# Kernel tuning notes

Measured on AMD Instinct MI355X. Metric: run time of the kernel, lower is better.

Reference implementation:

```python
import jax, jax.numpy as jnp
import numpy as np

B, S, D, H = 2, 2048, 1024, 16
DK = D // H

def setup_inputs() -> dict:
    key = jax.random.key(0)
    ks = jax.random.split(key, 11)
    scale = 1.0 / np.sqrt(D)
    inp = {
        'Q': jax.random.normal(ks[0], (B, S, D), jnp.float32),
        'K': jax.random.normal(ks[1], (B, S, D), jnp.float32),
        'V': jax.random.normal(ks[2], (B, S, D), jnp.float32),
        'Wq': jax.random.normal(ks[3], (D, D), jnp.float32) * scale,
        'bq': jax.random.normal(ks[4], (D,), jnp.float32) * 0.01,
        'Wk': jax.random.normal(ks[5], (D, D), jnp.float32) * scale,
        'bk': jax.random.normal(ks[6], (D,), jnp.float32) * 0.01,
        'Wv': jax.random.normal(ks[7], (D, D), jnp.float32) * scale,
        'bv': jax.random.normal(ks[8], (D,), jnp.float32) * 0.01,
        'Wo': jax.random.normal(ks[9], (D, D), jnp.float32) * scale,
        'bo': jax.random.normal(ks[10], (D,), jnp.float32) * 0.01,
    }
    return inp

def reference(Q, K, V, Wq, bq, Wk, bk, Wv, bv, Wo, bo):
    bs = Q.shape[0]
    # projections (torch Linear: x @ W.T + b), reshape to [b, h, s, d_k]
    q = (Q @ Wq.T + bq).reshape(bs, -1, H, DK).transpose(0, 2, 1, 3)
    k = (K @ Wk.T + bk).reshape(bs, -1, H, DK).transpose(0, 2, 1, 3)
    v = (V @ Wv.T + bv).reshape(bs, -1, H, DK).transpose(0, 2, 1, 3)
    # scaled dot-product attention (no mask, dropout p=0)
    scores = jnp.einsum('bhqd,bhkd->bhqk', q, k) / np.sqrt(DK).astype(np.float32)
    attn = jax.nn.softmax(scores, axis=-1)
    ctx = jnp.einsum('bhqk,bhkd->bhqd', attn, v)
    concat = ctx.transpose(0, 2, 1, 3).reshape(bs, -1, D)
    return concat @ Wo.T + bo
```

## Files before the change

### kernel.cpp

```cpp
#include <hip/hip_runtime.h>
#include <hip/hip_bf16.h>
#include <stdint.h>

#define B_  2
#define S_  2048
#define D_  1024
#define H_  16
#define DK_ 64
#define M_  (B_ * S_)

#define QSCALE 0.18033688011112042f

typedef __attribute__((ext_vector_type(4)))  float f32x4;
typedef __attribute__((ext_vector_type(16))) float f32x16;
typedef __attribute__((ext_vector_type(8)))  short bf16x8;

__device__ __forceinline__ unsigned short f2bf(float f) {
    union { float f; unsigned u; } a; a.f = f;
    unsigned u = a.u;
    unsigned r = (u + 0x7fffu + ((u >> 16) & 1u)) >> 16;
    return (unsigned short)r;
}
__device__ __forceinline__ unsigned pk2(float lo, float hi) {
    union { float f; unsigned u; } a, b; a.f = lo; b.f = hi;
    unsigned ra = a.u + 0x7fffu + ((a.u >> 16) & 1u);
    unsigned rb = b.u + 0x7fffu + ((b.u >> 16) & 1u);
    return __builtin_amdgcn_perm(rb, ra, 0x07060302u);
}
__device__ __forceinline__ unsigned pk2f(float lo, float hi) {
    union { float f; unsigned u; } a, b; a.f = lo; b.f = hi;
    return __builtin_amdgcn_perm(b.u + 0x8000u, a.u + 0x8000u, 0x07060302u);
}

__device__ __forceinline__ void gload16(const void* g, void* l) {
    __builtin_amdgcn_global_load_lds(
        (const __attribute__((address_space(1))) void*)g,
        (__attribute__((address_space(3))) void*)l, 16, 0, 0);
}

__global__ __launch_bounds__(256) void cvt_all(
    const float* __restrict__ p0, const float* __restrict__ p1,
    const float* __restrict__ p2, const float* __restrict__ p3,
    const float* __restrict__ p4, const float* __restrict__ p5,
    const float* __restrict__ p6,
    unsigned short* __restrict__ o0, unsigned short* __restrict__ o1,
    unsigned short* __restrict__ o2, unsigned short* __restrict__ o3,
    unsigned short* __restrict__ o4, unsigned short* __restrict__ o5,
    unsigned short* __restrict__ o6) {
    const int y = blockIdx.y;
    if (y >= 3 && blockIdx.x >= 512) return;
    const float* in = (y == 0) ? p0 : (y == 1) ? p1 : (y == 2) ? p2 :
                      (y == 3) ? p3 : (y == 4) ? p4 : (y == 5) ? p5 : p6;
    unsigned short* out = (y == 0) ? o0 : (y == 1) ? o1 : (y == 2) ? o2 :
                          (y == 3) ? o3 : (y == 4) ? o4 : (y == 5) ? o5 : o6;
    const int i = blockIdx.x * 256 + threadIdx.x;
    const float4* p = (const float4*)in + (size_t)i * 2;
    float4 u = p[0], v = p[1];
    union { unsigned us[4]; bf16x8 v; } o;
    o.us[0] = pk2(u.x, u.y); o.us[1] = pk2(u.z, u.w);
    o.us[2] = pk2(v.x, v.y); o.us[3] = pk2(v.z, v.w);
    *((bf16x8*)out + i) = o.v;
}

__device__ __forceinline__ void gemm128_core(const unsigned short* __restrict__ A,
                                             const unsigned short* __restrict__ Bw,
                                             char* sm,
                                             int brow, int bcol, f32x4 (&acc)[4][4]) {
    constexpr int K = D_;
    const int t = threadIdx.x;
    const int l = t & 63;
    const int l15 = l & 15, l4 = l >> 4;
    const int wr = (t >> 6) >> 1, wc = (t >> 6) & 1;

    const unsigned short* Ap = A + (size_t)(brow + (t >> 2)) * K + (t & 3) * 8;
    const unsigned short* Bp = Bw + (size_t)(bcol + (t >> 2)) * K + (t & 3) * 8;

    {
        char* d = sm + t * 16;
        gload16(Ap, d);
        gload16(Ap + 64 * K, d + 4096);
        gload16(Bp, d + 8192);
        gload16(Bp + 64 * K, d + 12288);
    }
    __syncthreads();

    unsigned sbuf = 0;
    for (int k0 = 0; k0 < K; k0 += 32) {
        if (k0 + 32 < K) {
            char* d = sm + (sbuf ^ 16384u) + t * 16;
            gload16(Ap + k0 + 32, d);
            gload16(Ap + 64 * K + k0 + 32, d + 4096);
            gload16(Bp + k0 + 32, d + 8192);
            gload16(Bp + 64 * K + k0 + 32, d + 12288);
        }

        const char* Ab = sm + sbuf;
        bf16x8 af[4], bfv[4];
#pragma unroll
        for (int m = 0; m < 4; m++)
            af[m] = *(const bf16x8*)(Ab + (wr * 64 + m * 16 + l15) * 64 + l4 * 16);
#pragma unroll
        for (int n = 0; n < 4; n++)
            bfv[n] = *(const bf16x8*)(Ab + 8192 + (wc * 64 + n * 16 + l15) * 64 + l4 * 16);
#pragma unroll
        for (int m = 0; m < 4; m++)
#pragma unroll
            for (int n = 0; n < 4; n++)
                acc[m][n] = __builtin_amdgcn_mfma_f32_16x16x32_bf16(af[m], bfv[n],
                                                                    acc[m][n], 0, 0, 0);

        if (k0 + 32 < K) __syncthreads();
        sbuf ^= 16384u;
    }
}

__global__ __launch_bounds__(256) void gemm_qkv(
    const unsigned short* __restrict__ xq, const unsigned short* __restrict__ xk,
    const unsigned short* __restrict__ xv,
    const unsigned short* __restrict__ wq, const unsigned short* __restrict__ wk,
    const unsigned short* __restrict__ wv,
    const float* __restrict__ bq, const float* __restrict__ bk,
    const float* __restrict__ bv,
    unsigned short* __restrict__ oq, unsigned short* __restrict__ ok,
    unsigned short* __restrict__ ov) {
    __shared__ char sm[32768];

    const int bid = blockIdx.x;
    const int wg = (bid & 7) * 96 + (bid >> 3);
    const int bx = wg & 7, by = (wg >> 3) & 31, z = wg >> 8;

    const unsigned short* A  = (z == 0) ? xq : (z == 1) ? xk : xv;
    const unsigned short* Bw = (z == 0) ? wq : (z == 1) ? wk : wv;
    const float* bias        = (z == 0) ? bq : (z == 1) ? bk : bv;
    unsigned short* out      = (z == 0) ? oq : (z == 1) ? ok : ov;

    const int brow = by * 128;
    const int bcol = bx * 128;
    const f32x4 zf = {0.0f, 0.0f, 0.0f, 0.0f};
    f32x4 acc[4][4];
#pragma unroll
    for (int i = 0; i < 4; i++)
#pragma unroll
        for (int j = 0; j < 4; j++) acc[i][j] = zf;

    gemm128_core(A, Bw, sm, brow, bcol, acc);

    const int t = threadIdx.x;
    const int l = t & 63;
    const int l15 = l & 15, l4 = l >> 4;
    const int wr = (t >> 6) >> 1, wc = (t >> 6) & 1;
    const float scale = (z == 0) ? QSCALE : 1.0f;

#pragma unroll
    for (int n = 0; n < 4; n++) {
        const int col = bcol + wc * 64 + n * 16 + l15;
        const float bia = bias[col];
        const int h = col >> 6, dk = col & 63;
#pragma unroll
        for (int m = 0; m < 4; m++) {
            const int row0 = brow + wr * 64 + m * 16 + l4 * 4;
            const int b = row0 >> 11, s0 = row0 & (S_ - 1);
            if (z != 2) {
#pragma unroll
                for (int r = 0; r < 4; r++) {
                    float v = (acc[m][n][r] + bia) * scale;
                    out[((size_t)((b * H_ + h) * S_ + (s0 + r))) * DK_ + dk] = f2bf(v);
                }
            } else {
                const int st_ = s0 >> 7, sl = s0 & 127;
                const int g = (sl >> 6) & 1, c = (sl >> 4) & 3;
                const int j2 = (sl >> 2) & 3;
                const int sig = ((j2 & 1) << 1) | (j2 >> 1);
                uint2 o;
                o.x = pk2(acc[m][n][0] + bia, acc[m][n][1] + bia);
                o.y = pk2(acc[m][n][2] + bia, acc[m][n][3] + bia);
                *(uint2*)((char*)out +
                          (((((size_t)(b * H_ + h) * 16 + st_) * 2 + g) * 4 + c) * 64 + dk) * 32 +
                          sig * 8) = o;
            }
        }
    }
}

__global__ __launch_bounds__(256) void gemm_out(const unsigned short* __restrict__ A,
                                                const unsigned short* __restrict__ Bw,
                                                const float* __restrict__ bias,
                                                float* __restrict__ out) {
    __shared__ char sm[32768];

    const int bid = blockIdx.x;
    const int wg = (bid & 7) * 32 + (bid >> 3);
    const int bx = wg & 7, by = wg >> 3;

    const int brow = by * 128;
    const int bcol = bx * 128;
    const f32x4 zf = {0.0f, 0.0f, 0.0f, 0.0f};
    f32x4 acc[4][4];
#pragma unroll
    for (int i = 0; i < 4; i++)
#pragma unroll
        for (int j = 0; j < 4; j++) acc[i][j] = zf;

    gemm128_core(A, Bw, sm, brow, bcol, acc);

    const int t = threadIdx.x;
    const int l = t & 63;
    const int l15 = l & 15, l4 = l >> 4;
    const int wr = (t >> 6) >> 1, wc = (t >> 6) & 1;
#pragma unroll
    for (int n = 0; n < 4; n++) {
        const int col = bcol + wc * 64 + n * 16 + l15;
        const float bia = bias[col];
#pragma unroll
        for (int m = 0; m < 4; m++) {
            const int row0 = brow + wr * 64 + m * 16 + l4 * 4;
#pragma unroll
            for (int r = 0; r < 4; r++)
                out[(size_t)(row0 + r) * D_ + col] = acc[m][n][r] + bia;
        }
    }
}

__global__ __launch_bounds__(512, 4) void attn_kernel(const unsigned short* __restrict__ qh,
                                                      const unsigned short* __restrict__ kh,
                                                      const unsigned short* __restrict__ vimg,
                                                      unsigned short* __restrict__ ctx) {
    __shared__ unsigned short smem[2][16384];
    char* smb = (char*)smem;

    const int t = threadIdx.x;
    const int w = t >> 6, l = t & 63;
    const int l31 = l & 31, hi = l >> 5;
    const int hi16 = hi * 16;
    const int grp = w >> 2;
    const int qs  = w & 3;

    const int bid = blockIdx.x;
    const int bh = (bid & 7) * 4 + ((bid >> 3) & 3);
    const int qt = bid >> 5;
    const int b = bh >> 4, h = bh & 15;

    const unsigned short* qg = qh + (size_t)bh * S_ * DK_;
    const unsigned short* kg = kh + (size_t)bh * S_ * DK_;

    const int q0 = qt * 128 + qs * 32;

    bf16x8 qf[4];
#pragma unroll
    for (int kc = 0; kc < 4; kc++)
        qf[kc] = *(const bf16x8*)(qg + (size_t)(q0 + l31) * DK_ + kc * 16 + hi * 8);

    const f32x16 zf16 = {0.0f};
    f32x16 acc0 = zf16, acc1 = zf16;
    float lpart = 0.0f;

    const int kc_ = t >> 7, key_ = (t >> 1) & 63, hi_ = t & 1;
    const unsigned short* ksrc = kg + key_ * DK_ + kc_ * 16 + hi_ * 8;
    const unsigned short* vsrc = vimg + (size_t)bh * (16 * 8192) + t * 8;

    {
        char* kd = smb + t * 16;
        gload16(ksrc, kd);
        gload16(ksrc + 4096, kd + 8192);
        gload16(vsrc, kd + 16384);
        gload16(vsrc + 4096, kd + 16384 + 8192);
        ksrc += 8192; vsrc += 8192;
    }
    __syncthreads();

    unsigned roff = grp * 8192 + l31 * 32 + hi16;
    unsigned pd = 32768 + (unsigned)t * 16;

    for (int j = 0; j < 16; ++j) {
        if (j < 15) {
            gload16(ksrc, smb + pd);
            gload16(ksrc + 4096, smb + pd + 8192);
            gload16(vsrc, smb + pd + 16384);
            gload16(vsrc + 4096, smb + pd + 16384 + 8192);
            ksrc += 8192; vsrc += 8192;
        }

        const char* Kb = smb + roff;

        f32x16 st0, st1;
        __builtin_amdgcn_s_setprio(1);
        {
            bf16x8 k0 = *(const bf16x8*)(Kb);
            bf16x8 k1 = *(const bf16x8*)(Kb + 1024);
            st0 = __builtin_amdgcn_mfma_f32_32x32x16_bf16(k0, qf[0], zf16, 0, 0, 0);
            st1 = __builtin_amdgcn_mfma_f32_32x32x16_bf16(k1, qf[0], zf16, 0, 0, 0);
        }
#pragma unroll
        for (int kc = 1; kc < 4; kc++) {
            bf16x8 k0 = *(const bf16x8*)(Kb + kc * 2048);
            bf16x8 k1 = *(const bf16x8*)(Kb + kc * 2048 + 1024);
            st0 = __builtin_amdgcn_mfma_f32_32x32x16_bf16(k0, qf[kc], st0, 0, 0, 0);
            st1 = __builtin_amdgcn_mfma_f32_32x32x16_bf16(k1, qf[kc], st1, 0, 0, 0);
        }
        __builtin_amdgcn_s_setprio(0);

#pragma unroll
        for (int i = 0; i < 16; i++) st0[i] = __builtin_amdgcn_exp2f(st0[i]);
#pragma unroll
        for (int i = 0; i < 16; i++) st1[i] = __builtin_amdgcn_exp2f(st1[i]);

        float sv[8];
#pragma unroll
        for (int i = 0; i < 8; i++) sv[i] = (st0[i] + st0[i + 8]) + (st1[i] + st1[i + 8]);
#pragma unroll
        for (int s = 4; s >= 1; s >>= 1)
#pragma unroll
            for (int i = 0; i < s; i++) sv[i] += sv[i + s];
        lpart += sv[0];

        bf16x8 pf[4];
        {
            union { unsigned u[4]; bf16x8 v; } pu;
            pu.u[0] = pk2f(st0[0], st0[1]);   pu.u[1] = pk2f(st0[2], st0[3]);
            pu.u[2] = pk2f(st0[4], st0[5]);   pu.u[3] = pk2f(st0[6], st0[7]);
            pf[0] = pu.v;
            pu.u[0] = pk2f(st0[8], st0[9]);   pu.u[1] = pk2f(st0[10], st0[11]);
            pu.u[2] = pk2f(st0[12], st0[13]); pu.u[3] = pk2f(st0[14], st0[15]);
            pf[1] = pu.v;
            pu.u[0] = pk2f(st1[0], st1[1]);   pu.u[1] = pk2f(st1[2], st1[3]);
            pu.u[2] = pk2f(st1[4], st1[5]);   pu.u[3] = pk2f(st1[6], st1[7]);
            pf[2] = pu.v;
            pu.u[0] = pk2f(st1[8], st1[9]);   pu.u[1] = pk2f(st1[10], st1[11]);
            pu.u[2] = pk2f(st1[12], st1[13]); pu.u[3] = pk2f(st1[14], st1[15]);
            pf[3] = pu.v;
        }

        const char* Vb = smb + roff;
        __builtin_amdgcn_s_setprio(1);
#pragma unroll
        for (int c = 0; c < 4; c++) {
            bf16x8 v0 = *(const bf16x8*)(Vb + 16384 + c * 2048);
            bf16x8 v1 = *(const bf16x8*)(Vb + 16384 + c * 2048 + 1024);
            acc0 = __builtin_amdgcn_mfma_f32_32x32x16_bf16(v0, pf[c], acc0, 0, 0, 0);
            acc1 = __builtin_amdgcn_mfma_f32_32x32x16_bf16(v1, pf[c], acc1, 0, 0, 0);
        }
        __builtin_amdgcn_s_setprio(0);

        if (j < 15) __syncthreads();
        roff ^= 32768;
        pd ^= 32768;
    }

    lpart += __shfl_xor(lpart, 32);
    __syncthreads();
    char* ab = smb + qs * 8192 + l31 * 256;
    const int msw = (l31 & 7) << 4;
    if (grp == 1) {
#pragma unroll
        for (int jj = 0; jj < 4; jj++) {
            f32x4 x0 = {acc0[4 * jj], acc0[4 * jj + 1], acc0[4 * jj + 2], acc0[4 * jj + 3]};
            f32x4 x1 = {acc1[4 * jj], acc1[4 * jj + 1], acc1[4 * jj + 2], acc1[4 * jj + 3]};
            *(f32x4*)(ab + ((jj * 32 + hi16) ^ msw)) = x0;
            *(f32x4*)(ab + (128 + ((jj * 32 + hi16) ^ msw))) = x1;
        }
        if (hi == 0)
            *(float*)(smb + 32768 + qs * 128 + l31 * 4) = lpart;
    }
    __syncthreads();
    if (grp == 0) {
        const float lB = *(const float*)(smb + 32768 + qs * 128 + l31 * 4);
        const float inv = 1.0f / (lpart + lB);
        unsigned short* op = ctx + ((size_t)b * S_ + (q0 + l31)) * D_ + h * 64;
#pragma unroll
        for (int jj = 0; jj < 4; jj++) {
            f32x4 b0 = *(const f32x4*)(ab + ((jj * 32 + hi16) ^ msw));
            f32x4 b1 = *(const f32x4*)(ab + (128 + ((jj * 32 + hi16) ^ msw)));
            uint2 o;
            o.x = pk2f((acc0[4 * jj + 0] + b0[0]) * inv, (acc0[4 * jj + 1] + b0[1]) * inv);
            o.y = pk2f((acc0[4 * jj + 2] + b0[2]) * inv, (acc0[4 * jj + 3] + b0[3]) * inv);
            *(uint2*)(op + jj * 8 + hi * 4) = o;
            o.x = pk2f((acc1[4 * jj + 0] + b1[0]) * inv, (acc1[4 * jj + 1] + b1[1]) * inv);
            o.y = pk2f((acc1[4 * jj + 2] + b1[2]) * inv, (acc1[4 * jj + 3] + b1[3]) * inv);
            *(uint2*)(op + 32 + jj * 8 + hi * 4) = o;
        }
    }
}

extern "C" void kernel_launch(void* const* d_in, const int* in_sizes, int n_in,
                              void* d_out, int out_size, void* d_ws, size_t ws_size,
                              hipStream_t stream) {
    const float* Q  = (const float*)d_in[0];
    const float* K  = (const float*)d_in[1];
    const float* V  = (const float*)d_in[2];
    const float* Wq = (const float*)d_in[3];
    const float* bq = (const float*)d_in[4];
    const float* Wk = (const float*)d_in[5];
    const float* bk = (const float*)d_in[6];
    const float* Wv = (const float*)d_in[7];
    const float* bv = (const float*)d_in[8];
    const float* Wo = (const float*)d_in[9];
    const float* bo = (const float*)d_in[10];

    const size_t NX = (size_t)M_ * D_;
    const size_t NW = (size_t)D_ * D_;

    unsigned short* ws = (unsigned short*)d_ws;
    unsigned short* xq  = ws; ws += NX;
    unsigned short* xk  = ws; ws += NX;
    unsigned short* xv  = ws; ws += NX;
    unsigned short* wqb = ws; ws += NW;
    unsigned short* wkb = ws; ws += NW;
    unsigned short* wvb = ws; ws += NW;
    unsigned short* wob = ws; ws += NW;
    unsigned short* qhb = ws; ws += NX;
    unsigned short* khb = ws; ws += NX;
    unsigned short* vip = ws; ws += NX;
    unsigned short* ctx = ws; ws += NX;

    cvt_all<<<dim3(2048, 7), 256, 0, stream>>>(Q, K, V, Wq, Wk, Wv, Wo,
                                               xq, xk, xv, wqb, wkb, wvb, wob);

    gemm_qkv<<<dim3(768), 256, 0, stream>>>(
        xq, xk, xv, wqb, wkb, wvb, bq, bk, bv, qhb, khb, vip);

    attn_kernel<<<dim3(512), 512, 0, stream>>>(qhb, khb, vip, ctx);

    gemm_out<<<dim3(256), 256, 0, stream>>>(ctx, wob, bo, (float*)d_out);
}
```

Before: 111.4 us.

## Rewrite QKV projection GEMM with 256x256 tiles and staged pipelined loads

```diff
diff --git a/kernel.cpp b/kernel.cpp
--- a/kernel.cpp
+++ b/kernel.cpp
@@ -62,6 +62,153 @@
     *((bf16x8*)out + i) = o.v;
 }
 
+template <int R, int C>
+__device__ __forceinline__ void qkv_phase(const char* bb, unsigned rA0, unsigned rB0,
+                                          f32x4 (&aq)[4][2]) {
+    bf16x8 af[4];
+    bf16x8 bf2[2];
+#pragma unroll
+    for (int m = 0; m < 4; m++)
+        af[m] = *(const bf16x8*)(bb + rA0 + R * 8192 + m * 256);
+#pragma unroll
+    for (int n = 0; n < 2; n++)
+        bf2[n] = *(const bf16x8*)(bb + rB0 + C * 8192 + n * 256);
+    __builtin_amdgcn_s_setprio(1);
+#pragma unroll
+    for (int m = 0; m < 4; m++)
+#pragma unroll
+        for (int n = 0; n < 2; n++)
+            aq[m][n] = __builtin_amdgcn_mfma_f32_16x16x32_bf16(af[m], bf2[n],
+                                                               aq[m][n], 0, 0, 0);
+    __builtin_amdgcn_s_setprio(0);
+}
+
+__global__ __launch_bounds__(512, 2) void gemm_qkv(
+    const unsigned short* __restrict__ xq, const unsigned short* __restrict__ xk,
+    const unsigned short* __restrict__ xv,
+    const unsigned short* __restrict__ wq, const unsigned short* __restrict__ wk,
+    const unsigned short* __restrict__ wv,
+    const float* __restrict__ bq, const float* __restrict__ bk,
+    const float* __restrict__ bv,
+    unsigned short* __restrict__ oq, unsigned short* __restrict__ ok,
+    unsigned short* __restrict__ ov) {
+    constexpr int K = D_;
+    __shared__ char sm[65536];
+    char* smd = sm;
+
+    const int bid = blockIdx.x;
+    const int wg = (bid & 7) * 24 + (bid >> 3);
+    const int z = wg >> 6;
+    const int rz = wg & 63;
+    const int by = rz >> 2, bx = rz & 3;
+    const int brow = by * 256, bcol = bx * 256;
+
+    const unsigned short* A  = (z == 0) ? xq : (z == 1) ? xk : xv;
+    const unsigned short* Bw = (z == 0) ? wq : (z == 1) ? wk : wv;
+    const float* bias        = (z == 0) ? bq : (z == 1) ? bk : bv;
+    unsigned short* out      = (z == 0) ? oq : (z == 1) ? ok : ov;
+
+    const int t = threadIdx.x;
+    const int l = t & 63, w = t >> 6;
+    const int l15 = l & 15, l4 = l >> 4;
+    const int wr2 = w >> 2, wc2 = w & 3;
+
+    const f32x4 zf = {0.0f, 0.0f, 0.0f, 0.0f};
+    f32x4 acc0[4][2], acc1[4][2], acc2[4][2], acc3[4][2];
+#pragma unroll
+    for (int m = 0; m < 4; m++)
+#pragma unroll
+        for (int n = 0; n < 2; n++) {
+            acc0[m][n] = zf; acc1[m][n] = zf; acc2[m][n] = zf; acc3[m][n] = zf;
+        }
+
+    const unsigned short* ApT = A + (size_t)(brow + (t & 127)) * K + (t >> 7) * 8;
+    const unsigned short* BpT = Bw + (size_t)(bcol + (t & 127)) * K + (t >> 7) * 8;
+    const unsigned dln = (unsigned)t * 16;
+
+    auto STAGE_A = [&](int h, int k0, unsigned buf) {
+        gload16(ApT + (size_t)h * 128 * K + k0, smd + buf + h * 8192 + dln);
+    };
+    auto STAGE_B = [&](int h, int k0, unsigned buf) {
+        gload16(BpT + (size_t)h * 128 * K + k0, smd + buf + 16384 + h * 8192 + dln);
+    };
+
+    const unsigned rA0 = (unsigned)((l4 * 128 + wr2 * 64 + l15) * 16);
+    const unsigned rB0 = 16384u + (unsigned)((l4 * 128 + wc2 * 32 + l15) * 16);
+
+    STAGE_A(0, 0, 0u); STAGE_B(0, 0, 0u); STAGE_A(1, 0, 0u); STAGE_B(1, 0, 0u);
+
+    constexpr int NT = K / 32;
+    for (int kt = 0; kt < NT; ++kt) {
+        const unsigned cur = (kt & 1) ? 32768u : 0u;
+        const unsigned nb = cur ^ 32768u;
+        const char* bb = smd + cur;
+        if (kt + 1 < NT) {
+            const int k1 = (kt + 1) * 32;
+            STAGE_A(0, k1, nb);
+            asm volatile("s_waitcnt vmcnt(3)\n\ts_barrier" ::: "memory");
+            __builtin_amdgcn_sched_barrier(0);
+            qkv_phase<0, 0>(bb, rA0, rB0, acc0);
+            STAGE_B(0, k1, nb);
+            asm volatile("s_waitcnt vmcnt(3)\n\ts_barrier" ::: "memory");
+            __builtin_amdgcn_sched_barrier(0);
+            qkv_phase<1, 0>(bb, rA0, rB0, acc1);
+            STAGE_A(1, k1, nb);
+            asm volatile("s_waitcnt vmcnt(3)\n\ts_barrier" ::: "memory");
+            __builtin_amdgcn_sched_barrier(0);
+            qkv_phase<0, 1>(bb, rA0, rB0, acc2);
+            STAGE_B(1, k1, nb);
+            asm volatile("s_barrier" ::: "memory");
+            __builtin_amdgcn_sched_barrier(0);
+            qkv_phase<1, 1>(bb, rA0, rB0, acc3);
+        } else {
+            asm volatile("s_waitcnt vmcnt(0)\n\ts_barrier" ::: "memory");
+            __builtin_amdgcn_sched_barrier(0);
+            qkv_phase<0, 0>(bb, rA0, rB0, acc0);
+            qkv_phase<1, 0>(bb, rA0, rB0, acc1);
+            qkv_phase<0, 1>(bb, rA0, rB0, acc2);
+            qkv_phase<1, 1>(bb, rA0, rB0, acc3);
+        }
+    }
+
+    const float scale = (z == 0) ? QSCALE : 1.0f;
+    auto epi = [&](f32x4 (&aq)[4][2], int R, int C) {
+#pragma unroll
+        for (int n = 0; n < 2; n++) {
+            const int col = bcol + C * 128 + wc2 * 32 + n * 16 + l15;
+            const float bia = bias[col];
+            const int h = col >> 6, dk = col & 63;
+#pragma unroll
+            for (int m = 0; m < 4; m++) {
+                const int row0 = brow + R * 128 + wr2 * 64 + m * 16 + l4 * 4;
+                const int b = row0 >> 11, s0 = row0 & (S_ - 1);
+                if (z != 2) {
+#pragma unroll
+                    for (int r = 0; r < 4; r++) {
+                        float v = (aq[m][n][r] + bia) * scale;
+                        out[((size_t)((b * H_ + h) * S_ + (s0 + r))) * DK_ + dk] = f2bf(v);
+                    }
+                } else {
+                    const int st_ = s0 >> 7, sl = s0 & 127;
+                    const int g = (sl >> 6) & 1, c = (sl >> 4) & 3;
+                    const int j2 = (sl >> 2) & 3;
+                    const int sig = ((j2 & 1) << 1) | (j2 >> 1);
+                    uint2 o;
+                    o.x = pk2(aq[m][n][0] + bia, aq[m][n][1] + bia);
+                    o.y = pk2(aq[m][n][2] + bia, aq[m][n][3] + bia);
+                    *(uint2*)((char*)out +
+                              (((((size_t)(b * H_ + h) * 16 + st_) * 2 + g) * 4 + c) * 64 + dk) * 32 +
+                              sig * 8) = o;
+                }
+            }
+        }
+    };
+    epi(acc0, 0, 0);
+    epi(acc1, 1, 0);
+    epi(acc2, 0, 1);
+    epi(acc3, 1, 1);
+}
+
 __device__ __forceinline__ void gemm128_core(const unsigned short* __restrict__ A,
                                              const unsigned short* __restrict__ Bw,
                                              char* sm,
@@ -111,74 +258,6 @@
 
         if (k0 + 32 < K) __syncthreads();
         sbuf ^= 16384u;
-    }
-}
-
-__global__ __launch_bounds__(256) void gemm_qkv(
-    const unsigned short* __restrict__ xq, const unsigned short* __restrict__ xk,
-    const unsigned short* __restrict__ xv,
-    const unsigned short* __restrict__ wq, const unsigned short* __restrict__ wk,
-    const unsigned short* __restrict__ wv,
-    const float* __restrict__ bq, const float* __restrict__ bk,
-    const float* __restrict__ bv,
-    unsigned short* __restrict__ oq, unsigned short* __restrict__ ok,
-    unsigned short* __restrict__ ov) {
-    __shared__ char sm[32768];
-
-    const int bid = blockIdx.x;
-    const int wg = (bid & 7) * 96 + (bid >> 3);
-    const int bx = wg & 7, by = (wg >> 3) & 31, z = wg >> 8;
-
-    const unsigned short* A  = (z == 0) ? xq : (z == 1) ? xk : xv;
-    const unsigned short* Bw = (z == 0) ? wq : (z == 1) ? wk : wv;
-    const float* bias        = (z == 0) ? bq : (z == 1) ? bk : bv;
-    unsigned short* out      = (z == 0) ? oq : (z == 1) ? ok : ov;
-
-    const int brow = by * 128;
-    const int bcol = bx * 128;
-    const f32x4 zf = {0.0f, 0.0f, 0.0f, 0.0f};
-    f32x4 acc[4][4];
-#pragma unroll
-    for (int i = 0; i < 4; i++)
-#pragma unroll
-        for (int j = 0; j < 4; j++) acc[i][j] = zf;
-
-    gemm128_core(A, Bw, sm, brow, bcol, acc);
-
-    const int t = threadIdx.x;
-    const int l = t & 63;
-    const int l15 = l & 15, l4 = l >> 4;
-    const int wr = (t >> 6) >> 1, wc = (t >> 6) & 1;
-    const float scale = (z == 0) ? QSCALE : 1.0f;
-
-#pragma unroll
-    for (int n = 0; n < 4; n++) {
-        const int col = bcol + wc * 64 + n * 16 + l15;
-        const float bia = bias[col];
-        const int h = col >> 6, dk = col & 63;
-#pragma unroll
-        for (int m = 0; m < 4; m++) {
-            const int row0 = brow + wr * 64 + m * 16 + l4 * 4;
-            const int b = row0 >> 11, s0 = row0 & (S_ - 1);
-            if (z != 2) {
-#pragma unroll
-                for (int r = 0; r < 4; r++) {
-                    float v = (acc[m][n][r] + bia) * scale;
-                    out[((size_t)((b * H_ + h) * S_ + (s0 + r))) * DK_ + dk] = f2bf(v);
-                }
-            } else {
-                const int st_ = s0 >> 7, sl = s0 & 127;
-                const int g = (sl >> 6) & 1, c = (sl >> 4) & 3;
-                const int j2 = (sl >> 2) & 3;
-                const int sig = ((j2 & 1) << 1) | (j2 >> 1);
-                uint2 o;
-                o.x = pk2(acc[m][n][0] + bia, acc[m][n][1] + bia);
-                o.y = pk2(acc[m][n][2] + bia, acc[m][n][3] + bia);
-                *(uint2*)((char*)out +
-                          (((((size_t)(b * H_ + h) * 16 + st_) * 2 + g) * 4 + c) * 64 + dk) * 32 +
-                          sig * 8) = o;
-            }
-        }
     }
 }
 
@@ -415,7 +494,7 @@
     cvt_all<<<dim3(2048, 7), 256, 0, stream>>>(Q, K, V, Wq, Wk, Wv, Wo,
                                                xq, xk, xv, wqb, wkb, wvb, wob);
 
-    gemm_qkv<<<dim3(768), 256, 0, stream>>>(
+    gemm_qkv<<<dim3(192), 512, 0, stream>>>(
         xq, xk, xv, wqb, wkb, wvb, bq, bk, bv, qhb, khb, vip);
 
     attn_kernel<<<dim3(512), 512, 0, stream>>>(qhb, khb, vip, ctx);
```

New measurement: 118.5 us. +6.4%, slower.

## Fuse fp32-to-bf16 conversion into GEMM tile loads and drop conversion kernel

Applied to the files above, without the earlier changes.

```diff
diff --git a/kernel.cpp b/kernel.cpp
--- a/kernel.cpp
+++ b/kernel.cpp
@@ -38,61 +38,76 @@
         (__attribute__((address_space(3))) void*)l, 16, 0, 0);
 }
 
-__global__ __launch_bounds__(256) void cvt_all(
-    const float* __restrict__ p0, const float* __restrict__ p1,
-    const float* __restrict__ p2, const float* __restrict__ p3,
-    const float* __restrict__ p4, const float* __restrict__ p5,
-    const float* __restrict__ p6,
-    unsigned short* __restrict__ o0, unsigned short* __restrict__ o1,
-    unsigned short* __restrict__ o2, unsigned short* __restrict__ o3,
-    unsigned short* __restrict__ o4, unsigned short* __restrict__ o5,
-    unsigned short* __restrict__ o6) {
-    const int y = blockIdx.y;
-    if (y >= 3 && blockIdx.x >= 512) return;
-    const float* in = (y == 0) ? p0 : (y == 1) ? p1 : (y == 2) ? p2 :
-                      (y == 3) ? p3 : (y == 4) ? p4 : (y == 5) ? p5 : p6;
-    unsigned short* out = (y == 0) ? o0 : (y == 1) ? o1 : (y == 2) ? o2 :
-                          (y == 3) ? o3 : (y == 4) ? o4 : (y == 5) ? o5 : o6;
-    const int i = blockIdx.x * 256 + threadIdx.x;
-    const float4* p = (const float4*)in + (size_t)i * 2;
-    float4 u = p[0], v = p[1];
-    union { unsigned us[4]; bf16x8 v; } o;
-    o.us[0] = pk2(u.x, u.y); o.us[1] = pk2(u.z, u.w);
-    o.us[2] = pk2(v.x, v.y); o.us[3] = pk2(v.z, v.w);
-    *((bf16x8*)out + i) = o.v;
-}
-
-__device__ __forceinline__ void gemm128_core(const unsigned short* __restrict__ A,
-                                             const unsigned short* __restrict__ Bw,
-                                             char* sm,
-                                             int brow, int bcol, f32x4 (&acc)[4][4]) {
+__device__ __forceinline__ bf16x8 pack8(const float4& a, const float4& b) {
+    union { unsigned u[4]; bf16x8 v; } p;
+    p.u[0] = pk2(a.x, a.y); p.u[1] = pk2(a.z, a.w);
+    p.u[2] = pk2(b.x, b.y); p.u[3] = pk2(b.z, b.w);
+    return p.v;
+}
+
+__global__ __launch_bounds__(256) void gemm_qkv(
+    const float* __restrict__ xq, const float* __restrict__ xk,
+    const float* __restrict__ xv,
+    const float* __restrict__ wq, const float* __restrict__ wk,
+    const float* __restrict__ wv,
+    const float* __restrict__ bq, const float* __restrict__ bk,
+    const float* __restrict__ bv,
+    unsigned short* __restrict__ oq, unsigned short* __restrict__ ok,
+    unsigned short* __restrict__ ov) {
     constexpr int K = D_;
+    __shared__ char sm[32768];
+
+    const int bid = blockIdx.x;
+    const int wg = (bid & 7) * 96 + (bid >> 3);
+    const int bx = wg & 7, by = (wg >> 3) & 31, z = wg >> 8;
+
+    const float* A  = (z == 0) ? xq : (z == 1) ? xk : xv;
+    const float* Bw = (z == 0) ? wq : (z == 1) ? wk : wv;
+    const float* bias = (z == 0) ? bq : (z == 1) ? bk : bv;
+    unsigned short* out = (z == 0) ? oq : (z == 1) ? ok : ov;
+
+    const int brow = by * 128;
+    const int bcol = bx * 128;
+    const f32x4 zf = {0.0f, 0.0f, 0.0f, 0.0f};
+    f32x4 acc[4][4];
+#pragma unroll
+    for (int i = 0; i < 4; i++)
+#pragma unroll
+        for (int j = 0; j < 4; j++) acc[i][j] = zf;
+
     const int t = threadIdx.x;
     const int l = t & 63;
     const int l15 = l & 15, l4 = l >> 4;
     const int wr = (t >> 6) >> 1, wc = (t >> 6) & 1;
 
-    const unsigned short* Ap = A + (size_t)(brow + (t >> 2)) * K + (t & 3) * 8;
-    const unsigned short* Bp = Bw + (size_t)(bcol + (t >> 2)) * K + (t & 3) * 8;
-
-    {
-        char* d = sm + t * 16;
-        gload16(Ap, d);
-        gload16(Ap + 64 * K, d + 4096);
-        gload16(Bp, d + 8192);
-        gload16(Bp + 64 * K, d + 12288);
-    }
+    const float* Ap0 = A + (size_t)(brow + (t >> 2)) * K + (t & 3) * 8;
+    const float* Ap1 = Ap0 + (size_t)64 * K;
+    const float* Bp0 = Bw + (size_t)(bcol + (t >> 2)) * K + (t & 3) * 8;
+    const float* Bp1 = Bp0 + (size_t)64 * K;
+
+    float4 r0a, r0b, r1a, r1b, r2a, r2b, r3a, r3b;
+    auto LOADREG = [&](int k0) {
+        r0a = *(const float4*)(Ap0 + k0); r0b = *(const float4*)(Ap0 + k0 + 4);
+        r1a = *(const float4*)(Ap1 + k0); r1b = *(const float4*)(Ap1 + k0 + 4);
+        r2a = *(const float4*)(Bp0 + k0); r2b = *(const float4*)(Bp0 + k0 + 4);
+        r3a = *(const float4*)(Bp1 + k0); r3b = *(const float4*)(Bp1 + k0 + 4);
+    };
+    auto CVTWRITE = [&](unsigned buf) {
+        char* d = sm + buf + t * 16;
+        *(bf16x8*)(d)         = pack8(r0a, r0b);
+        *(bf16x8*)(d + 4096)  = pack8(r1a, r1b);
+        *(bf16x8*)(d + 8192)  = pack8(r2a, r2b);
+        *(bf16x8*)(d + 12288) = pack8(r3a, r3b);
+    };
+
+    LOADREG(0);
+    CVTWRITE(0u);
     __syncthreads();
 
     unsigned sbuf = 0;
     for (int k0 = 0; k0 < K; k0 += 32) {
-        if (k0 + 32 < K) {
-            char* d = sm + (sbuf ^ 16384u) + t * 16;
-            gload16(Ap + k0 + 32, d);
-            gload16(Ap + 64 * K + k0 + 32, d + 4096);
-            gload16(Bp + k0 + 32, d + 8192);
-            gload16(Bp + 64 * K + k0 + 32, d + 12288);
-        }
+        const bool nx = (k0 + 32 < K);
+        if (nx) LOADREG(k0 + 32);
 
         const char* Ab = sm + sbuf;
         bf16x8 af[4], bfv[4];
@@ -109,48 +124,14 @@
                 acc[m][n] = __builtin_amdgcn_mfma_f32_16x16x32_bf16(af[m], bfv[n],
                                                                     acc[m][n], 0, 0, 0);
 
-        if (k0 + 32 < K) __syncthreads();
+        if (nx) {
+            CVTWRITE(sbuf ^ 16384u);
+            __syncthreads();
+        }
         sbuf ^= 16384u;
     }
-}
-
-__global__ __launch_bounds__(256) void gemm_qkv(
-    const unsigned short* __restrict__ xq, const unsigned short* __restrict__ xk,
-    const unsigned short* __restrict__ xv,
-    const unsigned short* __restrict__ wq, const unsigned short* __restrict__ wk,
-    const unsigned short* __restrict__ wv,
-    const float* __restrict__ bq, const float* __restrict__ bk,
-    const float* __restrict__ bv,
-    unsigned short* __restrict__ oq, unsigned short* __restrict__ ok,
-    unsigned short* __restrict__ ov) {
-    __shared__ char sm[32768];
-
-    const int bid = blockIdx.x;
-    const int wg = (bid & 7) * 96 + (bid >> 3);
-    const int bx = wg & 7, by = (wg >> 3) & 31, z = wg >> 8;
-
-    const unsigned short* A  = (z == 0) ? xq : (z == 1) ? xk : xv;
-    const unsigned short* Bw = (z == 0) ? wq : (z == 1) ? wk : wv;
-    const float* bias        = (z == 0) ? bq : (z == 1) ? bk : bv;
-    unsigned short* out      = (z == 0) ? oq : (z == 1) ? ok : ov;
-
-    const int brow = by * 128;
-    const int bcol = bx * 128;
-    const f32x4 zf = {0.0f, 0.0f, 0.0f, 0.0f};
-    f32x4 acc[4][4];
-#pragma unroll
-    for (int i = 0; i < 4; i++)
-#pragma unroll
-        for (int j = 0; j < 4; j++) acc[i][j] = zf;
-
-    gemm128_core(A, Bw, sm, brow, bcol, acc);
-
-    const int t = threadIdx.x;
-    const int l = t & 63;
-    const int l15 = l & 15, l4 = l >> 4;
-    const int wr = (t >> 6) >> 1, wc = (t >> 6) & 1;
+
     const float scale = (z == 0) ? QSCALE : 1.0f;
-
 #pragma unroll
     for (int n = 0; n < 4; n++) {
         const int col = bcol + wc * 64 + n * 16 + l15;
@@ -183,9 +164,10 @@
 }
 
 __global__ __launch_bounds__(256) void gemm_out(const unsigned short* __restrict__ A,
-                                                const unsigned short* __restrict__ Bw,
+                                                const float* __restrict__ Bw,
                                                 const float* __restrict__ bias,
                                                 float* __restrict__ out) {
+    constexpr int K = D_;
     __shared__ char sm[32768];
 
     const int bid = blockIdx.x;
@@ -201,12 +183,67 @@
 #pragma unroll
         for (int j = 0; j < 4; j++) acc[i][j] = zf;
 
-    gemm128_core(A, Bw, sm, brow, bcol, acc);
-
     const int t = threadIdx.x;
     const int l = t & 63;
     const int l15 = l & 15, l4 = l >> 4;
     const int wr = (t >> 6) >> 1, wc = (t >> 6) & 1;
+
+    const unsigned short* Ap = A + (size_t)(brow + (t >> 2)) * K + (t & 3) * 8;
+    const float* Bp0 = Bw + (size_t)(bcol + (t >> 2)) * K + (t & 3) * 8;
+    const float* Bp1 = Bp0 + (size_t)64 * K;
+
+    float4 r2a, r2b, r3a, r3b;
+    auto LOADB = [&](int k0) {
+        r2a = *(const float4*)(Bp0 + k0); r2b = *(const float4*)(Bp0 + k0 + 4);
+        r3a = *(const float4*)(Bp1 + k0); r3b = *(const float4*)(Bp1 + k0 + 4);
+    };
+    auto WRITEB = [&](unsigned buf) {
+        char* d = sm + buf + t * 16;
+        *(bf16x8*)(d + 8192)  = pack8(r2a, r2b);
+        *(bf16x8*)(d + 12288) = pack8(r3a, r3b);
+    };
+
+    {
+        char* d = sm + t * 16;
+        gload16(Ap, d);
+        gload16(Ap + (size_t)64 * K, d + 4096);
+        LOADB(0);
+        WRITEB(0u);
+    }
+    __syncthreads();
+
+    unsigned sbuf = 0;
+    for (int k0 = 0; k0 < K; k0 += 32) {
+        const bool nx = (k0 + 32 < K);
+        if (nx) {
+            char* d = sm + (sbuf ^ 16384u) + t * 16;
+            gload16(Ap + k0 + 32, d);
+            gload16(Ap + (size_t)64 * K + k0 + 32, d + 4096);
+            LOADB(k0 + 32);
+        }
+
+        const char* Ab = sm + sbuf;
+        bf16x8 af[4], bfv[4];
+#pragma unroll
+        for (int m = 0; m < 4; m++)
+            af[m] = *(const bf16x8*)(Ab + (wr * 64 + m * 16 + l15) * 64 + l4 * 16);
+#pragma unroll
+        for (int n = 0; n < 4; n++)
+            bfv[n] = *(const bf16x8*)(Ab + 8192 + (wc * 64 + n * 16 + l15) * 64 + l4 * 16);
+#pragma unroll
+        for (int m = 0; m < 4; m++)
+#pragma unroll
+            for (int n = 0; n < 4; n++)
+                acc[m][n] = __builtin_amdgcn_mfma_f32_16x16x32_bf16(af[m], bfv[n],
+                                                                    acc[m][n], 0, 0, 0);
+
+        if (nx) {
+            WRITEB(sbuf ^ 16384u);
+            __syncthreads();
+        }
+        sbuf ^= 16384u;
+    }
+
 #pragma unroll
     for (int n = 0; n < 4; n++) {
         const int col = bcol + wc * 64 + n * 16 + l15;
@@ -397,28 +434,17 @@
     const float* bo = (const float*)d_in[10];
 
     const size_t NX = (size_t)M_ * D_;
-    const size_t NW = (size_t)D_ * D_;
 
     unsigned short* ws = (unsigned short*)d_ws;
-    unsigned short* xq  = ws; ws += NX;
-    unsigned short* xk  = ws; ws += NX;
-    unsigned short* xv  = ws; ws += NX;
-    unsigned short* wqb = ws; ws += NW;
-    unsigned short* wkb = ws; ws += NW;
-    unsigned short* wvb = ws; ws += NW;
-    unsigned short* wob = ws; ws += NW;
     unsigned short* qhb = ws; ws += NX;
     unsigned short* khb = ws; ws += NX;
     unsigned short* vip = ws; ws += NX;
     unsigned short* ctx = ws; ws += NX;
 
-    cvt_all<<<dim3(2048, 7), 256, 0, stream>>>(Q, K, V, Wq, Wk, Wv, Wo,
-                                               xq, xk, xv, wqb, wkb, wvb, wob);
-
     gemm_qkv<<<dim3(768), 256, 0, stream>>>(
-        xq, xk, xv, wqb, wkb, wvb, bq, bk, bv, qhb, khb, vip);
+        Q, K, V, Wq, Wk, Wv, bq, bk, bv, qhb, khb, vip);
 
     attn_kernel<<<dim3(512), 512, 0, stream>>>(qhb, khb, vip, ctx);
 
-    gemm_out<<<dim3(256), 256, 0, stream>>>(ctx, wob, bo, (float*)d_out);
-}
+    gemm_out<<<dim3(256), 256, 0, stream>>>(ctx, Wo, bo, (float*)d_out);
+}
```

Result: slower. 143.5 us (+28.8%).
